# Performance work log

Hardware: AMD Instinct MI355X
Metric: run time of the kernel (lower is better)

Reference implementation:

```python
import jax, jax.numpy as jnp
import numpy as np

# dims
BS = 4096
MOVE = 4
N_EN, ED = 64, 16
N_AL, AD = 63, 16
OTHER = 20
MF = MOVE + OTHER            # m_f_size = 24
IN = MOVE + N_EN * ED + N_AL * AD + OTHER  # 2056
H = 4                        # n_head
HE = 128                     # hypernet_emb
E = 64                       # attention_dim (emb_dim)
NA = N_EN + N_AL + 1         # n_agents = 128
RNN = 256
EN_START = MOVE
AL_START = MOVE + N_EN * ED
OTH_START = AL_START + N_AL * AD


def setup_inputs() -> dict:
    key = jax.random.key(0)
    ks = jax.random.split(key, 32)
    g = lambda k, shape: (jax.random.normal(k, shape, dtype=jnp.float32) * 0.05)
    return {
        "obs": jax.random.normal(ks[0], (BS, IN), dtype=jnp.float32),
        # per-head query MLP (Linear(MF,HE)+ReLU+Linear(HE,E,no bias)), stacked over heads
        "Wq1": g(ks[1], (H, HE, MF)), "bq1": g(ks[2], (H, HE)), "Wq2": g(ks[3], (H, E, HE)),
        # per-head key_m MLP
        "Wkm1": g(ks[4], (H, HE, MF)), "bkm1": g(ks[5], (H, HE)), "Wkm2": g(ks[6], (H, E, HE)),
        # per-head entity key linears (no bias)
        "Wke": g(ks[7], (H, E, ED)), "Wka": g(ks[8], (H, E, AD)),
        # per-head value_m MLP
        "Wvm1": g(ks[9], (H, HE, MF)), "bvm1": g(ks[10], (H, HE)), "Wvm2": g(ks[11], (H, E, HE)),
        # per-head entity value linears (no bias)
        "Wve": g(ks[12], (H, E, ED)), "Wva": g(ks[13], (H, E, AD)),
        # b net: Linear(IN,E)+ReLU+Linear(E,1)
        "Wb1": g(ks[14], (E, IN)), "bb1": g(ks[15], (E,)), "Wb2": g(ks[16], (1, E)), "bb2": g(ks[17], (1,)),
        # hyper_w_head: Linear(IN,HE)+ReLU+Linear(HE,H)
        "Wh1": g(ks[18], (HE, IN)), "bh1": g(ks[19], (HE,)), "Wh2": g(ks[20], (H, HE)), "bh2": g(ks[21], (H,)),
        # final layer: Linear(E*NA, RNN)
        "Wf": g(ks[22], (RNN, E * NA)), "bf": g(ks[23], (RNN,)),
    }


def _headed_mlp(x, W1, b1, W2):
    # x: [B, MF]; W1: [H, HE, MF]; W2: [H, E, HE] -> [B, H, E]
    h = jax.nn.relu(jnp.einsum("bf,hgf->bhg", x, W1) + b1[None])
    return jnp.einsum("bhg,heg->bhe", h, W2)


def reference(obs, Wq1, bq1, Wq2, Wkm1, bkm1, Wkm2, Wke, Wka,
              Wvm1, bvm1, Wvm2, Wve, Wva, Wb1, bb1, Wb2, bb2,
              Wh1, bh1, Wh2, bh2, Wf, bf):
    bs = obs.shape[0]
    m = jnp.concatenate([obs[:, :MOVE], obs[:, OTH_START:]], axis=1)        # [B, MF]
    enemies = obs[:, EN_START:AL_START].reshape(bs, N_EN, ED)               # [B, N_EN, ED]
    allies = obs[:, AL_START:OTH_START].reshape(bs, N_AL, AD)               # [B, N_AL, AD]

    q = _headed_mlp(m, Wq1, bq1, Wq2)                                       # [B, H, E]
    km = _headed_mlp(m, Wkm1, bkm1, Wkm2)[:, :, None, :]                    # [B, H, 1, E]
    ke = jnp.einsum("bnd,hed->bhne", enemies, Wke)                          # [B, H, N_EN, E]
    ka = jnp.einsum("bnd,hed->bhne", allies, Wka)                           # [B, H, N_AL, E]
    k = jnp.concatenate([km, ke, ka], axis=2)                               # [B, H, NA, E]

    vm = _headed_mlp(m, Wvm1, bvm1, Wvm2)[:, :, None, :]
    ve = jnp.einsum("bnd,hed->bhne", enemies, Wve)
    va = jnp.einsum("bnd,hed->bhne", allies, Wva)
    v = jnp.concatenate([vm, ve, va], axis=2)                               # [B, H, NA, E]

    logits = jnp.einsum("bhe,bhne->bhn", q, k) / np.sqrt(E).astype(np.float32)
    w = jax.nn.softmax(logits, axis=-1)                                     # [B, H, NA]
    # torch: atten_w (B,1,NA) expanded to (B,E,NA) * v permuted to (B,E,NA); flatten [E,NA]
    scores = (w[:, :, None, :] * jnp.swapaxes(v, 2, 3)).reshape(bs, H, E * NA)

    b_term = jax.nn.relu(obs @ Wb1.T + bb1) @ Wb2.T + bb2                   # [B, 1]
    w_head = jnp.abs(jax.nn.relu(obs @ Wh1.T + bh1) @ Wh2.T + bh2)          # [B, H]
    mixed = jnp.einsum("bhk,bh->bk", scores, w_head) + b_term               # [B, E*NA]
    return mixed @ Wf.T + bf                                                # [B, RNN]
```

## Files before the change

### kernel.cpp

```cpp
#include <hip/hip_runtime.h>
#include <hip/hip_bf16.h>

typedef __attribute__((ext_vector_type(8))) short short8;
typedef __attribute__((ext_vector_type(4))) float floatx4;

#define NIN 2056
#define KPAD 2080
#define NBS 4096

__device__ __forceinline__ void gl_lds16(const ushort* g, ushort* l) {
#if defined(__has_builtin) && __has_builtin(__builtin_amdgcn_global_load_lds)
  __builtin_amdgcn_global_load_lds(
      (const __attribute__((address_space(1))) unsigned int*)g,
      (__attribute__((address_space(3))) unsigned int*)l, 16, 0, 0);
#else
  *(uint4*)l = *(const uint4*)g;
#endif
}

__device__ __forceinline__ float wsum(float v) {
#pragma unroll
  for (int o = 32; o; o >>= 1) v += __shfl_xor(v, o, 64);
  return v;
}
__device__ __forceinline__ float wmax(float v) {
#pragma unroll
  for (int o = 32; o; o >>= 1) v = fmaxf(v, __shfl_xor(v, o, 64));
  return v;
}

__global__ void prep_small(const float* __restrict__ obs,
                           const float* __restrict__ Wb1, const float* __restrict__ Wh1,
                           const float* __restrict__ Wq1, const float* __restrict__ Wkm1,
                           const float* __restrict__ Wvm1, const float* __restrict__ bq1,
                           const float* __restrict__ bkm1, const float* __restrict__ bvm1,
                           const float* __restrict__ Wq2, const float* __restrict__ Wkm2,
                           const float* __restrict__ Wvm2,
                           __hip_bfloat16* __restrict__ mmat,
                           __hip_bfloat16* __restrict__ w1cat,
                           __hip_bfloat16* __restrict__ w1m, float* __restrict__ b1cat,
                           __hip_bfloat16* __restrict__ w2cat) {
  int bid = blockIdx.x, tid = threadIdx.x;
  if (bid < 512) {
    int idx = bid * 256 + tid;
    int b = idx >> 5, j = idx & 31;
    float v = 0.f;
    if (j < 4) v = obs[(size_t)b * NIN + j];
    else if (j < 24) v = obs[(size_t)b * NIN + 2032 + j];
    mmat[idx] = __float2bfloat16(v);
  } else if (bid < 704) {
    int r = bid - 512;
    const float* src = (r < 64) ? (Wb1 + (size_t)r * NIN) : (Wh1 + (size_t)(r - 64) * NIN);
    for (int j = tid; j < KPAD; j += 256)
      w1cat[(size_t)r * KPAD + j] = __float2bfloat16(j < NIN ? src[j] : 0.f);
  } else if (bid < 896) {
    int idx = (bid - 704) * 256 + tid;
    int row = idx >> 5, j = idx & 31;
    int net = row >> 9, hg = row & 511;
    const float* W1 = net == 0 ? Wq1 : (net == 1 ? Wkm1 : Wvm1);
    float v = (j < 24) ? W1[(size_t)hg * 24 + j] : 0.f;
    w1m[idx] = __float2bfloat16(v);
    if (j == 0) {
      const float* b1 = net == 0 ? bq1 : (net == 1 ? bkm1 : bvm1);
      b1cat[row] = b1[hg];
    }
  } else {
    int idx = (bid - 896) * 256 + tid;
    int row = idx >> 7, g = idx & 127;
    int net = row >> 8, he = row & 255;
    const float* W2 = net == 0 ? Wq2 : (net == 1 ? Wkm2 : Wvm2);
    w2cat[idx] = __float2bfloat16(W2[(size_t)he * 128 + g]);
  }
}

__global__ void p6a_twf(const float* __restrict__ Wf, float* __restrict__ Wft,
                        float* __restrict__ rowsum) {
  __shared__ float t[64][65];
  int kt = blockIdx.x, rt = blockIdx.y;
  int tid = threadIdx.x;
  int kl = tid & 63, r0 = tid >> 6;
#pragma unroll
  for (int ii = 0; ii < 16; ++ii) {
    int rl = ii * 4 + r0;
    t[rl][kl] = Wf[(size_t)(rt * 64 + rl) * 8192 + kt * 64 + kl];
  }
  __syncthreads();
#pragma unroll
  for (int ii = 0; ii < 16; ++ii) {
    int kl2 = ii * 4 + r0;
    Wft[(size_t)(kt * 64 + kl2) * 256 + rt * 64 + kl] = t[kl][kl2];
  }
  if (tid < 64) {
    float s = 0.f;
    for (int kk = 0; kk < 64; ++kk) s += t[tid][kk];
    atomicAdd(&rowsum[rt * 64 + tid], s);
  }
}

__global__ void p6b_yt(const float* __restrict__ Wft, const float* __restrict__ Wve,
                       const float* __restrict__ Wva, __hip_bfloat16* __restrict__ Yt) {
  int n = blockIdx.x;
  int r = threadIdx.x;
  if (n == 0) {
    alignas(16) __hip_bfloat16 tmp[8];
    for (int e0 = 0; e0 < 64; e0 += 8) {
#pragma unroll
      for (int j = 0; j < 8; ++j)
        tmp[j] = __float2bfloat16(Wft[(size_t)((e0 + j) * 128) * 256 + r]);
      *(uint4*)(Yt + (size_t)r * 8192 + 8128 + e0) = *(const uint4*)tmp;
    }
    return;
  }
  const float* Wv = (n <= 64) ? Wve : Wva;
  float accv[64];
#pragma unroll
  for (int j = 0; j < 64; ++j) accv[j] = 0.f;
  for (int e = 0; e < 64; ++e) {
    float v = Wft[(size_t)(e * 128 + n) * 256 + r];
#pragma unroll
    for (int hd = 0; hd < 64; ++hd)
      accv[hd] += Wv[(hd >> 4) * 1024 + e * 16 + (hd & 15)] * v;
  }
#pragma unroll
  for (int c = 0; c < 8; ++c) {
    alignas(16) __hip_bfloat16 tmp[8];
#pragma unroll
    for (int j = 0; j < 8; ++j) tmp[j] = __float2bfloat16(accv[c * 8 + j]);
    *(uint4*)(Yt + (size_t)r * 8192 + (n - 1) * 64 + c * 8) = *(const uint4*)tmp;
  }
}

__global__ __launch_bounds__(256) void qkv_fused(
    const __hip_bfloat16* __restrict__ mmat_, const __hip_bfloat16* __restrict__ w1m_,
    const float* __restrict__ b1cat, const __hip_bfloat16* __restrict__ w2cat_,
    float* __restrict__ QKV) {
  __shared__ alignas(16) ushort lH[64 * 136];
  const ushort* mmat = (const ushort*)mmat_;
  const ushort* w1m = (const ushort*)w1m_;
  const ushort* w2cat = (const ushort*)w2cat_;
  int mt = blockIdx.x, z = blockIdx.y;
  int t = threadIdx.x;
  int w = t >> 6, l = t & 63, r16 = l & 15, kg = l >> 4;
  floatx4 zero4 = {0.f, 0.f, 0.f, 0.f};
  short8 a1 = *(const short8*)(mmat + (size_t)(mt * 64 + w * 16 + r16) * 32 + kg * 8);
  floatx4 acc1[8];
#pragma unroll
  for (int c = 0; c < 8; ++c) {
    short8 b1 = *(const short8*)(w1m + (size_t)(z * 128 + c * 16 + r16) * 32 + kg * 8);
    acc1[c] = __builtin_amdgcn_mfma_f32_16x16x32_bf16(a1, b1, zero4, 0, 0, 0);
  }
#pragma unroll
  for (int c = 0; c < 8; ++c) {
    int col = c * 16 + r16;
    float bias = b1cat[z * 128 + col];
#pragma unroll
    for (int r = 0; r < 4; ++r) {
      float v = acc1[c][r] + bias;
      v = v > 0.f ? v : 0.f;
      __hip_bfloat16 bv = __float2bfloat16(v);
      lH[(w * 16 + kg * 4 + r) * 136 + col] = *(ushort*)&bv;
    }
  }
  __syncthreads();
  floatx4 acc2[4] = {zero4, zero4, zero4, zero4};
#pragma unroll
  for (int ks = 0; ks < 4; ++ks) {
    short8 a = *(const short8*)(lH + (w * 16 + r16) * 136 + ks * 32 + kg * 8);
#pragma unroll
    for (int c = 0; c < 4; ++c) {
      short8 b = *(const short8*)(w2cat + (size_t)(z * 64 + c * 16 + r16) * 128 + ks * 32 + kg * 8);
      acc2[c] = __builtin_amdgcn_mfma_f32_16x16x32_bf16(a, b, acc2[c], 0, 0, 0);
    }
  }
  float* Q = QKV + (size_t)(mt * 64) * 768 + z * 64;
#pragma unroll
  for (int c = 0; c < 4; ++c)
#pragma unroll
    for (int r = 0; r < 4; ++r)
      Q[(size_t)(w * 16 + kg * 4 + r) * 768 + c * 16 + r16] = acc2[c][r];
}

__global__ __launch_bounds__(256) void gemm_h1(
    const float* __restrict__ obs, const __hip_bfloat16* __restrict__ w1cat_,
    float* __restrict__ H1p) {
  __shared__ alignas(16) ushort lA[64 * 40];
  __shared__ alignas(16) ushort lB[64 * 40];
  const ushort* w1cat = (const ushort*)w1cat_;
  int mt = blockIdx.x, nt = blockIdx.y, z = blockIdx.z;
  int t = threadIdx.x;
  int w = t >> 6, l = t & 63, r16 = l & 15, kg = l >> 4;
  int srow = t >> 2, sc = (t & 3) * 8;
  int k0 = z * 512;
  const float* ga = obs + (size_t)(mt * 64 + srow) * NIN + k0 + sc;
  const ushort* gb = w1cat + (size_t)(nt * 64 + srow) * KPAD + k0 + sc;
  ushort* sa = lA + srow * 40 + sc;
  ushort* sb = lB + srow * 40 + sc;
  const ushort* fa = lA + (w * 16 + r16) * 40 + kg * 8;
  const ushort* fb0 = lB + r16 * 40 + kg * 8;
  floatx4 zero4 = {0.f, 0.f, 0.f, 0.f};
  floatx4 acc[4] = {zero4, zero4, zero4, zero4};
  int nK = (z == 3) ? 17 : 16;
  for (int ks = 0; ks < nK; ++ks) {
    float4 f0, f1;
    uint4 vb;
    bool tail = (ks == 16);
    if (!tail || (t & 3) == 0) {
      f0 = *(const float4*)(ga + ks * 32);
      f1 = *(const float4*)(ga + ks * 32 + 4);
    } else {
      f0 = make_float4(0.f, 0.f, 0.f, 0.f);
      f1 = make_float4(0.f, 0.f, 0.f, 0.f);
    }
    vb = *(const uint4*)(gb + ks * 32);
    __syncthreads();
    alignas(16) __hip_bfloat16 tmp[8];
    tmp[0] = __float2bfloat16(f0.x); tmp[1] = __float2bfloat16(f0.y);
    tmp[2] = __float2bfloat16(f0.z); tmp[3] = __float2bfloat16(f0.w);
    tmp[4] = __float2bfloat16(f1.x); tmp[5] = __float2bfloat16(f1.y);
    tmp[6] = __float2bfloat16(f1.z); tmp[7] = __float2bfloat16(f1.w);
    *(uint4*)sa = *(const uint4*)tmp;
    *(uint4*)sb = vb;
    __syncthreads();
    short8 a = *(const short8*)fa;
#pragma unroll
    for (int c = 0; c < 4; ++c) {
      short8 bb = *(const short8*)(fb0 + c * 16 * 40);
      acc[c] = __builtin_amdgcn_mfma_f32_16x16x32_bf16(a, bb, acc[c], 0, 0, 0);
    }
  }
  int row0 = mt * 64 + w * 16 + kg * 4;
  int col0 = nt * 64 + r16;
  float* C = H1p + (size_t)z * NBS * 192;
#pragma unroll
  for (int c = 0; c < 4; ++c)
#pragma unroll
    for (int r = 0; r < 4; ++r)
      C[(size_t)(row0 + r) * 192 + col0 + c * 16] = acc[c][r];
}

__global__ __launch_bounds__(256) void gemm_final(
    const ushort* __restrict__ Xg, const ushort* __restrict__ Yt,
    float* __restrict__ part) {
  __shared__ alignas(16) ushort lA[128 * 32];
  __shared__ alignas(16) ushort lB[128 * 32];
  int bid = blockIdx.x;
  int z = bid & 7, nt = (bid >> 3) & 1, mt = bid >> 4;
  int t = threadIdx.x;
  int w = t >> 6, l = t & 63, r16 = l & 15, kg = l >> 4;
  int wr = (w >> 1) * 64, wc = (w & 1) * 64;
  const ushort* ga0 = Xg + (size_t)(mt * 128 + (t >> 2)) * 8192 + z * 1024 + (t & 3) * 8;
  const ushort* ga1 = ga0 + (size_t)64 * 8192;
  const ushort* gb0 = Yt + (size_t)(nt * 128 + (t >> 2)) * 8192 + z * 1024 + (t & 3) * 8;
  const ushort* gb1 = gb0 + (size_t)64 * 8192;
  ushort* la0 = lA + t * 8;
  ushort* la1 = lA + 2048 + t * 8;
  ushort* lb0 = lB + t * 8;
  ushort* lb1 = lB + 2048 + t * 8;
  const ushort* fa0 = lA + (wr + r16) * 32 + kg * 8;
  const ushort* fb0 = lB + (wc + r16) * 32 + kg * 8;
  floatx4 zero4 = {0.f, 0.f, 0.f, 0.f};
  floatx4 acc[4][4];
#pragma unroll
  for (int i = 0; i < 4; ++i)
#pragma unroll
    for (int j = 0; j < 4; ++j) acc[i][j] = zero4;
  for (int ks = 0; ks < 32; ++ks) {
    gl_lds16(ga0, la0);
    gl_lds16(ga1, la1);
    gl_lds16(gb0, lb0);
    gl_lds16(gb1, lb1);
    ga0 += 32; ga1 += 32; gb0 += 32; gb1 += 32;
    __syncthreads();
    short8 a[4], b[4];
#pragma unroll
    for (int mi = 0; mi < 4; ++mi) a[mi] = *(const short8*)(fa0 + mi * 512);
#pragma unroll
    for (int ni = 0; ni < 4; ++ni) b[ni] = *(const short8*)(fb0 + ni * 512);
#pragma unroll
    for (int mi = 0; mi < 4; ++mi)
#pragma unroll
      for (int ni = 0; ni < 4; ++ni)
        acc[mi][ni] = __builtin_amdgcn_mfma_f32_16x16x32_bf16(a[mi], b[ni], acc[mi][ni], 0, 0, 0);
    __syncthreads();
  }
  int row0 = mt * 128 + wr + kg * 4;
  int col0 = nt * 128 + wc + r16;
  float* cp = part + (size_t)z * NBS * 256;
#pragma unroll
  for (int mi = 0; mi < 4; ++mi)
#pragma unroll
    for (int ni = 0; ni < 4; ++ni)
#pragma unroll
      for (int r = 0; r < 4; ++r)
        cp[(size_t)(row0 + mi * 16 + r) * 256 + col0 + ni * 16] = acc[mi][ni][r];
}

__global__ __launch_bounds__(256) void row_kernel(
    const float* __restrict__ obs, const float* __restrict__ QKV,
    const float* __restrict__ H1p, const float* __restrict__ Wke,
    const float* __restrict__ Wka, const float* __restrict__ Wb2,
    const float* __restrict__ bb2, const float* __restrict__ Wh2,
    const float* __restrict__ bh2, const float* __restrict__ bb1,
    const float* __restrict__ bh1, __hip_bfloat16* __restrict__ X,
    float* __restrict__ bterm) {
  __shared__ float q_lds[4][256];
  __shared__ float qke_lds[4][64], qka_lds[4][64];
  int wv = threadIdx.x >> 6;
  int lane = threadIdx.x & 63;
  int b = blockIdx.x * 4 + wv;
  const float* qkv = QKV + (size_t)b * 768;
  float q_h[4], km_h[4], vm_h[4];
#pragma unroll
  for (int h = 0; h < 4; ++h) {
    q_h[h] = qkv[h * 64 + lane];
    km_h[h] = qkv[256 + h * 64 + lane];
    vm_h[h] = qkv[512 + h * 64 + lane];
    q_lds[wv][h * 64 + lane] = q_h[h];
  }
  __syncthreads();
  {
    int h = lane >> 4, d = lane & 15;
    float se = 0.f, sa = 0.f;
    for (int e = 0; e < 64; ++e) {
      float qv = q_lds[wv][h * 64 + e];
      se += qv * Wke[h * 1024 + e * 16 + d];
      sa += qv * Wka[h * 1024 + e * 16 + d];
    }
    qke_lds[wv][lane] = se;
    qka_lds[wv][lane] = sa;
  }
  __syncthreads();
  float l0[4];
#pragma unroll
  for (int h = 0; h < 4; ++h) l0[h] = wsum(q_h[h] * km_h[h]) * 0.125f;
  const float* ob = obs + (size_t)b * NIN;
  alignas(16) float en[16];
  alignas(16) float al[16];
  {
    const float4* ep = (const float4*)(ob + 4 + lane * 16);
    const float4* ap = (const float4*)(ob + 1028 + lane * 16);
#pragma unroll
    for (int i = 0; i < 4; ++i) {
      *(float4*)(en + 4 * i) = ep[i];
      *(float4*)(al + 4 * i) = ap[i];
    }
  }
  bool av = lane < 63;
  float lE[4], lA_[4];
#pragma unroll
  for (int h = 0; h < 4; ++h) {
    float sE = 0.f, sA = 0.f;
#pragma unroll
    for (int d = 0; d < 16; ++d) {
      sE += en[d] * qke_lds[wv][h * 16 + d];
      sA += al[d] * qka_lds[wv][h * 16 + d];
    }
    lE[h] = sE * 0.125f;
    lA_[h] = sA * 0.125f;
  }
  const float* h1p = H1p + (size_t)b * 192;
  const size_t S1 = (size_t)NBS * 192;
  float vb0 = h1p[lane] + h1p[S1 + lane] + h1p[2 * S1 + lane] + h1p[3 * S1 + lane];
  float vw0 = h1p[64 + lane] + h1p[S1 + 64 + lane] + h1p[2 * S1 + 64 + lane] + h1p[3 * S1 + 64 + lane];
  float vw1 = h1p[128 + lane] + h1p[S1 + 128 + lane] + h1p[2 * S1 + 128 + lane] + h1p[3 * S1 + 128 + lane];
  float hb = fmaxf(vb0 + bb1[lane], 0.f);
  float bt = wsum(hb * Wb2[lane]) + bb2[0];
  float hw0 = fmaxf(vw0 + bh1[lane], 0.f);
  float hw1 = fmaxf(vw1 + bh1[64 + lane], 0.f);
  float whead[4];
#pragma unroll
  for (int h = 0; h < 4; ++h)
    whead[h] = fabsf(wsum(hw0 * Wh2[h * 128 + lane] + hw1 * Wh2[h * 128 + 64 + lane]) + bh2[h]);
  float wE[4], wA[4], w0[4];
#pragma unroll
  for (int h = 0; h < 4; ++h) {
    float mE = wmax(lE[h]);
    float mA = wmax(av ? lA_[h] : -3.0e38f);
    float mx = fmaxf(fmaxf(mE, mA), l0[h]);
    float pE = __expf(lE[h] - mx);
    float pA = av ? __expf(lA_[h] - mx) : 0.f;
    float p0 = __expf(l0[h] - mx);
    float den = wsum(pE + pA) + p0;
    float s = whead[h] / den;
    wE[h] = pE * s;
    wA[h] = pA * s;
    w0[h] = p0 * s;
  }
  __hip_bfloat16* xr = X + (size_t)b * 8192;
#pragma unroll
  for (int h = 0; h < 4; ++h) {
    alignas(16) __hip_bfloat16 tmp[16];
#pragma unroll
    for (int d = 0; d < 16; ++d) tmp[d] = __float2bfloat16(wE[h] * en[d]);
    uint4* dst = (uint4*)(xr + (size_t)lane * 64 + h * 16);
    dst[0] = ((const uint4*)tmp)[0];
    dst[1] = ((const uint4*)tmp)[1];
  }
  if (av) {
#pragma unroll
    for (int h = 0; h < 4; ++h) {
      alignas(16) __hip_bfloat16 tmp[16];
#pragma unroll
      for (int d = 0; d < 16; ++d) tmp[d] = __float2bfloat16(wA[h] * al[d]);
      uint4* dst = (uint4*)(xr + (size_t)(64 + lane) * 64 + h * 16);
      dst[0] = ((const uint4*)tmp)[0];
      dst[1] = ((const uint4*)tmp)[1];
    }
  }
  float x0 = w0[0] * vm_h[0] + w0[1] * vm_h[1] + w0[2] * vm_h[2] + w0[3] * vm_h[3];
  xr[8128 + lane] = __float2bfloat16(x0);
  if (lane == 0) bterm[b] = bt;
}

__global__ void k7_out(const float* __restrict__ part, const float* __restrict__ bterm,
                       const float* __restrict__ rowsum, const float* __restrict__ bfv,
                       float* __restrict__ out) {
  int b = blockIdx.x, r = threadIdx.x;
  size_t i = (size_t)b * 256 + r;
  const size_t S = (size_t)NBS * 256;
  float v = 0.f;
#pragma unroll
  for (int z = 0; z < 8; ++z) v += part[i + z * S];
  out[i] = v + bterm[b] * rowsum[r] + bfv[r];
}

extern "C" void kernel_launch(void* const* d_in, const int* in_sizes, int n_in,
                              void* d_out, int out_size, void* d_ws, size_t ws_size,
                              hipStream_t stream) {
  const float* obs = (const float*)d_in[0];
  const float* Wq1 = (const float*)d_in[1];
  const float* bq1 = (const float*)d_in[2];
  const float* Wq2 = (const float*)d_in[3];
  const float* Wkm1 = (const float*)d_in[4];
  const float* bkm1 = (const float*)d_in[5];
  const float* Wkm2 = (const float*)d_in[6];
  const float* Wke = (const float*)d_in[7];
  const float* Wka = (const float*)d_in[8];
  const float* Wvm1 = (const float*)d_in[9];
  const float* bvm1 = (const float*)d_in[10];
  const float* Wvm2 = (const float*)d_in[11];
  const float* Wve = (const float*)d_in[12];
  const float* Wva = (const float*)d_in[13];
  const float* Wb1 = (const float*)d_in[14];
  const float* bb1 = (const float*)d_in[15];
  const float* Wb2 = (const float*)d_in[16];
  const float* bb2 = (const float*)d_in[17];
  const float* Wh1 = (const float*)d_in[18];
  const float* bh1 = (const float*)d_in[19];
  const float* Wh2 = (const float*)d_in[20];
  const float* bh2 = (const float*)d_in[21];
  const float* Wf = (const float*)d_in[22];
  const float* bfv = (const float*)d_in[23];
  float* out = (float*)d_out;

  char* ws = (char*)d_ws;
  size_t off = 0;
  auto alloc = [&](size_t bytes) -> void* {
    void* p = ws + off;
    off += (bytes + 255) & ~(size_t)255;
    return p;
  };
  __hip_bfloat16* mmat = (__hip_bfloat16*)alloc((size_t)NBS * 32 * 2);
  __hip_bfloat16* w1m = (__hip_bfloat16*)alloc((size_t)1536 * 32 * 2);
  float* b1cat = (float*)alloc(1536 * 4);
  __hip_bfloat16* w2cat = (__hip_bfloat16*)alloc((size_t)768 * 128 * 2);
  __hip_bfloat16* w1cat = (__hip_bfloat16*)alloc((size_t)192 * KPAD * 2);
  float* rowsum = (float*)alloc(256 * 4);
  float* bterm = (float*)alloc(NBS * 4);
  float* Wft = (float*)alloc((size_t)8192 * 256 * 4);
  __hip_bfloat16* Yt = (__hip_bfloat16*)alloc((size_t)256 * 8192 * 2);
  __hip_bfloat16* X = (__hip_bfloat16*)alloc((size_t)NBS * 8192 * 2);
  char* R = (char*)alloc((size_t)34 * 1024 * 1024);
  float* QKV = (float*)R;
  float* H1p = (float*)(R + (size_t)NBS * 768 * 4);
  float* part8 = (float*)R;

  hipMemsetAsync(rowsum, 0, 256 * 4, stream);

  prep_small<<<1280, 256, 0, stream>>>(obs, Wb1, Wh1, Wq1, Wkm1, Wvm1, bq1, bkm1, bvm1,
                                       Wq2, Wkm2, Wvm2, mmat, w1cat, w1m, b1cat, w2cat);
  p6a_twf<<<dim3(128, 4), 256, 0, stream>>>(Wf, Wft, rowsum);
  p6b_yt<<<128, 256, 0, stream>>>(Wft, Wve, Wva, Yt);

  gemm_h1<<<dim3(64, 3, 4), 256, 0, stream>>>(obs, w1cat, H1p);
  qkv_fused<<<dim3(64, 12), 256, 0, stream>>>(mmat, w1m, b1cat, w2cat, QKV);
  row_kernel<<<NBS / 4, 256, 0, stream>>>(obs, QKV, H1p, Wke, Wka, Wb2, bb2, Wh2, bh2,
                                          bb1, bh1, X, bterm);
  gemm_final<<<512, 256, 0, stream>>>((const ushort*)X, (const ushort*)Yt, part8);
  k7_out<<<NBS, 256, 0, stream>>>(part8, bterm, rowsum, bfv, out);

  (void)in_sizes; (void)n_in; (void)out_size; (void)ws_size;
}
```

Measured before the change: 271.1 us.

## Move q·Wk projections to MFMA, widen h1 GEMM tiles, coalesce X writes via head-major layout

The per-row q·Wke/q·Wka projections move out of the row kernel's scalar loop into the qkv_fused kernel as bf16 MFMAs. They use pre-transposed Wk tables built in the prep kernel and write QKE/QKA buffers. gemm_h1 now computes all 192 output columns per block, so obs is read once instead of three times. The X and Yt layouts are permuted to head-major, and row_kernel stages writes through LDS to emit coalesced 16-byte stores. The trade-offs are lower q·Wk precision from bf16 rounding, extra buffers, and fewer gemm_h1 blocks with more accumulator registers.

```diff
diff --git a/kernel.cpp b/kernel.cpp
--- a/kernel.cpp
+++ b/kernel.cpp
@@ -36,10 +36,13 @@
                            const float* __restrict__ bkm1, const float* __restrict__ bvm1,
                            const float* __restrict__ Wq2, const float* __restrict__ Wkm2,
                            const float* __restrict__ Wvm2,
+                           const float* __restrict__ Wke, const float* __restrict__ Wka,
                            __hip_bfloat16* __restrict__ mmat,
                            __hip_bfloat16* __restrict__ w1cat,
                            __hip_bfloat16* __restrict__ w1m, float* __restrict__ b1cat,
-                           __hip_bfloat16* __restrict__ w2cat) {
+                           __hip_bfloat16* __restrict__ w2cat,
+                           __hip_bfloat16* __restrict__ wket,
+                           __hip_bfloat16* __restrict__ wkat) {
   int bid = blockIdx.x, tid = threadIdx.x;
   if (bid < 512) {
     int idx = bid * 256 + tid;
@@ -64,12 +67,20 @@
       const float* b1 = net == 0 ? bq1 : (net == 1 ? bkm1 : bvm1);
       b1cat[row] = b1[hg];
     }
-  } else {
+  } else if (bid < 1280) {
     int idx = (bid - 896) * 256 + tid;
     int row = idx >> 7, g = idx & 127;
     int net = row >> 8, he = row & 255;
     const float* W2 = net == 0 ? Wq2 : (net == 1 ? Wkm2 : Wvm2);
     w2cat[idx] = __float2bfloat16(W2[(size_t)he * 128 + g]);
+  } else {
+    const float* W = (bid == 1280) ? Wke : Wka;
+    __hip_bfloat16* dst = (bid == 1280) ? wket : wkat;
+    for (int j = tid; j < 4096; j += 256) {
+      int e = j & 63, hd = j >> 6;
+      int h = hd >> 4, d = hd & 15;
+      dst[j] = __float2bfloat16(W[h * 1024 + e * 16 + d]);
+    }
   }
 }
 
@@ -107,7 +118,8 @@
 #pragma unroll
       for (int j = 0; j < 8; ++j)
         tmp[j] = __float2bfloat16(Wft[(size_t)((e0 + j) * 128) * 256 + r]);
-      *(uint4*)(Yt + (size_t)r * 8192 + 8128 + e0) = *(const uint4*)tmp;
+      *(uint4*)(Yt + (size_t)r * 8192 + (e0 >> 4) * 2048 + 2032 + (e0 & 15)) =
+          *(const uint4*)tmp;
     }
     return;
   }
@@ -126,18 +138,23 @@
     alignas(16) __hip_bfloat16 tmp[8];
 #pragma unroll
     for (int j = 0; j < 8; ++j) tmp[j] = __float2bfloat16(accv[c * 8 + j]);
-    *(uint4*)(Yt + (size_t)r * 8192 + (n - 1) * 64 + c * 8) = *(const uint4*)tmp;
+    *(uint4*)(Yt + (size_t)r * 8192 + (c >> 1) * 2048 + (size_t)(n - 1) * 16 + (c & 1) * 8) =
+        *(const uint4*)tmp;
   }
 }
 
 __global__ __launch_bounds__(256) void qkv_fused(
     const __hip_bfloat16* __restrict__ mmat_, const __hip_bfloat16* __restrict__ w1m_,
     const float* __restrict__ b1cat, const __hip_bfloat16* __restrict__ w2cat_,
-    float* __restrict__ QKV) {
+    const __hip_bfloat16* __restrict__ wket_, const __hip_bfloat16* __restrict__ wkat_,
+    float* __restrict__ QKV, float* __restrict__ QKE, float* __restrict__ QKA) {
   __shared__ alignas(16) ushort lH[64 * 136];
+  __shared__ alignas(16) ushort lq[64 * 72];
   const ushort* mmat = (const ushort*)mmat_;
   const ushort* w1m = (const ushort*)w1m_;
   const ushort* w2cat = (const ushort*)w2cat_;
+  const ushort* wket = (const ushort*)wket_;
+  const ushort* wkat = (const ushort*)wkat_;
   int mt = blockIdx.x, z = blockIdx.y;
   int t = threadIdx.x;
   int w = t >> 6, l = t & 63, r16 = l & 15, kg = l >> 4;
@@ -178,31 +195,56 @@
 #pragma unroll
     for (int r = 0; r < 4; ++r)
       Q[(size_t)(w * 16 + kg * 4 + r) * 768 + c * 16 + r16] = acc2[c][r];
+  if (z < 4) {
+#pragma unroll
+    for (int c = 0; c < 4; ++c)
+#pragma unroll
+      for (int r = 0; r < 4; ++r) {
+        __hip_bfloat16 bv = __float2bfloat16(acc2[c][r]);
+        lq[(w * 16 + kg * 4 + r) * 72 + c * 16 + r16] = *(ushort*)&bv;
+      }
+    short8 a0 = *(const short8*)(lq + (w * 16 + r16) * 72 + kg * 8);
+    short8 a1q = *(const short8*)(lq + (w * 16 + r16) * 72 + 32 + kg * 8);
+    const ushort* bke = wket + (size_t)(z * 16 + r16) * 64 + kg * 8;
+    const ushort* bka = wkat + (size_t)(z * 16 + r16) * 64 + kg * 8;
+    short8 bk0 = *(const short8*)bke;
+    short8 bk1 = *(const short8*)(bke + 32);
+    short8 ba0 = *(const short8*)bka;
+    short8 ba1 = *(const short8*)(bka + 32);
+    floatx4 ke = __builtin_amdgcn_mfma_f32_16x16x32_bf16(a0, bk0, zero4, 0, 0, 0);
+    ke = __builtin_amdgcn_mfma_f32_16x16x32_bf16(a1q, bk1, ke, 0, 0, 0);
+    floatx4 ka = __builtin_amdgcn_mfma_f32_16x16x32_bf16(a0, ba0, zero4, 0, 0, 0);
+    ka = __builtin_amdgcn_mfma_f32_16x16x32_bf16(a1q, ba1, ka, 0, 0, 0);
+#pragma unroll
+    for (int r = 0; r < 4; ++r) {
+      size_t row = (size_t)(mt * 64 + w * 16 + kg * 4 + r);
+      QKE[row * 64 + z * 16 + r16] = ke[r];
+      QKA[row * 64 + z * 16 + r16] = ka[r];
+    }
+  }
 }
 
 __global__ __launch_bounds__(256) void gemm_h1(
     const float* __restrict__ obs, const __hip_bfloat16* __restrict__ w1cat_,
     float* __restrict__ H1p) {
   __shared__ alignas(16) ushort lA[64 * 40];
-  __shared__ alignas(16) ushort lB[64 * 40];
+  __shared__ alignas(16) ushort lB[192 * 40];
   const ushort* w1cat = (const ushort*)w1cat_;
-  int mt = blockIdx.x, nt = blockIdx.y, z = blockIdx.z;
+  int mt = blockIdx.x, z = blockIdx.y;
   int t = threadIdx.x;
   int w = t >> 6, l = t & 63, r16 = l & 15, kg = l >> 4;
   int srow = t >> 2, sc = (t & 3) * 8;
   int k0 = z * 512;
   const float* ga = obs + (size_t)(mt * 64 + srow) * NIN + k0 + sc;
-  const ushort* gb = w1cat + (size_t)(nt * 64 + srow) * KPAD + k0 + sc;
   ushort* sa = lA + srow * 40 + sc;
-  ushort* sb = lB + srow * 40 + sc;
   const ushort* fa = lA + (w * 16 + r16) * 40 + kg * 8;
-  const ushort* fb0 = lB + r16 * 40 + kg * 8;
   floatx4 zero4 = {0.f, 0.f, 0.f, 0.f};
-  floatx4 acc[4] = {zero4, zero4, zero4, zero4};
+  floatx4 acc[12];
+#pragma unroll
+  for (int c = 0; c < 12; ++c) acc[c] = zero4;
   int nK = (z == 3) ? 17 : 16;
   for (int ks = 0; ks < nK; ++ks) {
     float4 f0, f1;
-    uint4 vb;
     bool tail = (ks == 16);
     if (!tail || (t & 3) == 0) {
       f0 = *(const float4*)(ga + ks * 32);
@@ -211,7 +253,10 @@
       f0 = make_float4(0.f, 0.f, 0.f, 0.f);
       f1 = make_float4(0.f, 0.f, 0.f, 0.f);
     }
-    vb = *(const uint4*)(gb + ks * 32);
+    uint4 vb[3];
+#pragma unroll
+    for (int i = 0; i < 3; ++i)
+      vb[i] = *(const uint4*)(w1cat + (size_t)(i * 64 + srow) * KPAD + k0 + sc + ks * 32);
     __syncthreads();
     alignas(16) __hip_bfloat16 tmp[8];
     tmp[0] = __float2bfloat16(f0.x); tmp[1] = __float2bfloat16(f0.y);
@@ -219,23 +264,24 @@
     tmp[4] = __float2bfloat16(f1.x); tmp[5] = __float2bfloat16(f1.y);
     tmp[6] = __float2bfloat16(f1.z); tmp[7] = __float2bfloat16(f1.w);
     *(uint4*)sa = *(const uint4*)tmp;
-    *(uint4*)sb = vb;
+#pragma unroll
+    for (int i = 0; i < 3; ++i)
+      *(uint4*)(lB + (i * 64 + srow) * 40 + sc) = vb[i];
     __syncthreads();
     short8 a = *(const short8*)fa;
 #pragma unroll
-    for (int c = 0; c < 4; ++c) {
-      short8 bb = *(const short8*)(fb0 + c * 16 * 40);
+    for (int c = 0; c < 12; ++c) {
+      short8 bb = *(const short8*)(lB + (c * 16 + r16) * 40 + kg * 8);
       acc[c] = __builtin_amdgcn_mfma_f32_16x16x32_bf16(a, bb, acc[c], 0, 0, 0);
     }
   }
+  float* C = H1p + (size_t)z * NBS * 192;
   int row0 = mt * 64 + w * 16 + kg * 4;
-  int col0 = nt * 64 + r16;
-  float* C = H1p + (size_t)z * NBS * 192;
-#pragma unroll
-  for (int c = 0; c < 4; ++c)
+#pragma unroll
+  for (int c = 0; c < 12; ++c)
 #pragma unroll
     for (int r = 0; r < 4; ++r)
-      C[(size_t)(row0 + r) * 192 + col0 + c * 16] = acc[c][r];
+      C[(size_t)(row0 + r) * 192 + c * 16 + r16] = acc[c][r];
 }
 
 __global__ __launch_bounds__(256) void gemm_final(
@@ -297,17 +343,19 @@
 
 __global__ __launch_bounds__(256) void row_kernel(
     const float* __restrict__ obs, const float* __restrict__ QKV,
-    const float* __restrict__ H1p, const float* __restrict__ Wke,
-    const float* __restrict__ Wka, const float* __restrict__ Wb2,
+    const float* __restrict__ QKE, const float* __restrict__ QKA,
+    const float* __restrict__ H1p, const float* __restrict__ Wb2,
     const float* __restrict__ bb2, const float* __restrict__ Wh2,
     const float* __restrict__ bh2, const float* __restrict__ bb1,
     const float* __restrict__ bh1, __hip_bfloat16* __restrict__ X,
     float* __restrict__ bterm) {
-  __shared__ float q_lds[4][256];
   __shared__ float qke_lds[4][64], qka_lds[4][64];
+  __shared__ uint4 xstage[4][2][256];
   int wv = threadIdx.x >> 6;
   int lane = threadIdx.x & 63;
   int b = blockIdx.x * 4 + wv;
+  qke_lds[wv][lane] = QKE[(size_t)b * 64 + lane];
+  qka_lds[wv][lane] = QKA[(size_t)b * 64 + lane];
   const float* qkv = QKV + (size_t)b * 768;
   float q_h[4], km_h[4], vm_h[4];
 #pragma unroll
@@ -315,21 +363,7 @@
     q_h[h] = qkv[h * 64 + lane];
     km_h[h] = qkv[256 + h * 64 + lane];
     vm_h[h] = qkv[512 + h * 64 + lane];
-    q_lds[wv][h * 64 + lane] = q_h[h];
-  }
-  __syncthreads();
-  {
-    int h = lane >> 4, d = lane & 15;
-    float se = 0.f, sa = 0.f;
-    for (int e = 0; e < 64; ++e) {
-      float qv = q_lds[wv][h * 64 + e];
-      se += qv * Wke[h * 1024 + e * 16 + d];
-      sa += qv * Wka[h * 1024 + e * 16 + d];
-    }
-    qke_lds[wv][lane] = se;
-    qka_lds[wv][lane] = sa;
-  }
-  __syncthreads();
+  }
   float l0[4];
 #pragma unroll
   for (int h = 0; h < 4; ++h) l0[h] = wsum(q_h[h] * km_h[h]) * 0.125f;
@@ -389,26 +423,32 @@
   __hip_bfloat16* xr = X + (size_t)b * 8192;
 #pragma unroll
   for (int h = 0; h < 4; ++h) {
-    alignas(16) __hip_bfloat16 tmp[16];
-#pragma unroll
-    for (int d = 0; d < 16; ++d) tmp[d] = __float2bfloat16(wE[h] * en[d]);
-    uint4* dst = (uint4*)(xr + (size_t)lane * 64 + h * 16);
-    dst[0] = ((const uint4*)tmp)[0];
-    dst[1] = ((const uint4*)tmp)[1];
-  }
-  if (av) {
-#pragma unroll
-    for (int h = 0; h < 4; ++h) {
-      alignas(16) __hip_bfloat16 tmp[16];
-#pragma unroll
-      for (int d = 0; d < 16; ++d) tmp[d] = __float2bfloat16(wA[h] * al[d]);
-      uint4* dst = (uint4*)(xr + (size_t)(64 + lane) * 64 + h * 16);
-      dst[0] = ((const uint4*)tmp)[0];
-      dst[1] = ((const uint4*)tmp)[1];
+    int buf = h & 1;
+    uint ue[8], ua[8];
+#pragma unroll
+    for (int j = 0; j < 8; ++j) {
+      __hip_bfloat16 lo = __float2bfloat16(wE[h] * en[2 * j]);
+      __hip_bfloat16 hi = __float2bfloat16(wE[h] * en[2 * j + 1]);
+      ue[j] = (uint)*(ushort*)&lo | ((uint)*(ushort*)&hi << 16);
+      __hip_bfloat16 alo = __float2bfloat16(wA[h] * al[2 * j]);
+      __hip_bfloat16 ahi = __float2bfloat16(wA[h] * al[2 * j + 1]);
+      ua[j] = (uint)*(ushort*)&alo | ((uint)*(ushort*)&ahi << 16);
+    }
+    xstage[wv][buf][lane * 2] = make_uint4(ue[0], ue[1], ue[2], ue[3]);
+    xstage[wv][buf][lane * 2 + 1] = make_uint4(ue[4], ue[5], ue[6], ue[7]);
+    if (av) {
+      xstage[wv][buf][(64 + lane) * 2] = make_uint4(ua[0], ua[1], ua[2], ua[3]);
+      xstage[wv][buf][(64 + lane) * 2 + 1] = make_uint4(ua[4], ua[5], ua[6], ua[7]);
+    }
+#pragma unroll
+    for (int s = 0; s < 4; ++s) {
+      uint4 v = xstage[wv][buf][s * 64 + lane];
+      if (!(s == 3 && lane >= 62))
+        *(uint4*)(xr + h * 2048 + s * 512 + lane * 8) = v;
     }
   }
   float x0 = w0[0] * vm_h[0] + w0[1] * vm_h[1] + w0[2] * vm_h[2] + w0[3] * vm_h[3];
-  xr[8128 + lane] = __float2bfloat16(x0);
+  xr[(lane >> 4) * 2048 + 2032 + (lane & 15)] = __float2bfloat16(x0);
   if (lane == 0) bterm[b] = bt;
 }
 
@@ -465,8 +505,12 @@
   float* b1cat = (float*)alloc(1536 * 4);
   __hip_bfloat16* w2cat = (__hip_bfloat16*)alloc((size_t)768 * 128 * 2);
   __hip_bfloat16* w1cat = (__hip_bfloat16*)alloc((size_t)192 * KPAD * 2);
+  __hip_bfloat16* wket = (__hip_bfloat16*)alloc(4096 * 2);
+  __hip_bfloat16* wkat = (__hip_bfloat16*)alloc(4096 * 2);
   float* rowsum = (float*)alloc(256 * 4);
   float* bterm = (float*)alloc(NBS * 4);
+  float* QKE = (float*)alloc((size_t)NBS * 64 * 4);
+  float* QKA = (float*)alloc((size_t)NBS * 64 * 4);
   float* Wft = (float*)alloc((size_t)8192 * 256 * 4);
   __hip_bfloat16* Yt = (__hip_bfloat16*)alloc((size_t)256 * 8192 * 2);
   __hip_bfloat16* X = (__hip_bfloat16*)alloc((size_t)NBS * 8192 * 2);
@@ -477,14 +521,16 @@
 
   hipMemsetAsync(rowsum, 0, 256 * 4, stream);
 
-  prep_small<<<1280, 256, 0, stream>>>(obs, Wb1, Wh1, Wq1, Wkm1, Wvm1, bq1, bkm1, bvm1,
-                                       Wq2, Wkm2, Wvm2, mmat, w1cat, w1m, b1cat, w2cat);
+  prep_small<<<1282, 256, 0, stream>>>(obs, Wb1, Wh1, Wq1, Wkm1, Wvm1, bq1, bkm1, bvm1,
+                                       Wq2, Wkm2, Wvm2, Wke, Wka,
+                                       mmat, w1cat, w1m, b1cat, w2cat, wket, wkat);
   p6a_twf<<<dim3(128, 4), 256, 0, stream>>>(Wf, Wft, rowsum);
   p6b_yt<<<128, 256, 0, stream>>>(Wft, Wve, Wva, Yt);
 
-  gemm_h1<<<dim3(64, 3, 4), 256, 0, stream>>>(obs, w1cat, H1p);
-  qkv_fused<<<dim3(64, 12), 256, 0, stream>>>(mmat, w1m, b1cat, w2cat, QKV);
-  row_kernel<<<NBS / 4, 256, 0, stream>>>(obs, QKV, H1p, Wke, Wka, Wb2, bb2, Wh2, bh2,
+  gemm_h1<<<dim3(64, 4), 256, 0, stream>>>(obs, w1cat, H1p);
+  qkv_fused<<<dim3(64, 12), 256, 0, stream>>>(mmat, w1m, b1cat, w2cat, wket, wkat,
+                                              QKV, QKE, QKA);
+  row_kernel<<<NBS / 4, 256, 0, stream>>>(obs, QKV, QKE, QKA, H1p, Wb2, bb2, Wh2, bh2,
                                           bb1, bh1, X, bterm);
   gemm_final<<<512, 256, 0, stream>>>((const ushort*)X, (const ushort*)Yt, part8);
   k7_out<<<NBS, 256, 0, stream>>>(part8, bterm, rowsum, bfv, out);
```

Measured after the change: 264.1 us. 1.03x faster.
